# Optimization experiments

Hardware: AMD Instinct MI355X
Metric: run time of the kernel (lower is better)

The kernel has to match this reference:

```python
import jax, jax.numpy as jnp
import numpy as np

K = 1.0      # Lorentz curvature param (geoopt convention: <x,x>_L = -K)
SQK = 1.0    # sqrt(K)
B, LOOKBACK, SEG, D = 256, 4096, 32, 256
N = LOOKBACK // SEG  # 128 segments


def _mink_inner(x, y):
    # Minkowski inner product, keepdims on last axis
    return -x[..., :1] * y[..., :1] + jnp.sum(x[..., 1:] * y[..., 1:], axis=-1, keepdims=True)


def _expmap0_spatial(v):
    # v: [..., D] spatial tangent at origin -> point on hyperboloid [..., D+1]
    n = jnp.linalg.norm(v, axis=-1, keepdims=True)
    ns = jnp.maximum(n, 1e-9)
    x0 = SQK * jnp.cosh(n / SQK)
    xr = SQK * jnp.sinh(n / SQK) * v / ns
    return jnp.concatenate([x0, xr], axis=-1)


def _projx(x):
    # re-project onto hyperboloid: x0 = sqrt(K + ||x_spatial||^2)
    xr = x[..., 1:]
    x0 = jnp.sqrt(K + jnp.sum(xr * xr, axis=-1, keepdims=True))
    return jnp.concatenate([x0, xr], axis=-1)


def _origin_like(x):
    return jnp.zeros_like(x).at[..., 0].set(SQK)


def _logmap(x, y):
    # log_x(y) on the Lorentz manifold
    alpha = jnp.maximum(-_mink_inner(x, y) / K, 1.0 + 1e-7)
    dist = SQK * jnp.arccosh(alpha)
    u = y - alpha * x  # tangent direction (unnormalized)
    un = jnp.sqrt(jnp.maximum(_mink_inner(u, u), 1e-12))
    return dist * u / un


def _expmap(x, u):
    # exp_x(u) on the Lorentz manifold
    un = jnp.sqrt(jnp.maximum(_mink_inner(u, u), 1e-12))
    theta = un / SQK
    return jnp.cosh(theta) * x + jnp.sinh(theta) * SQK * u / un


def _clip_norm(v, max_norm):
    # euclidean-norm clip (torch.norm semantics in source)
    n = jnp.linalg.norm(v, axis=-1, keepdims=True)
    return v / jnp.maximum(n, 1e-12) * jnp.minimum(n, max_norm)


def _encode(x, W, b):
    # [B, lookback] -> [B, N, D]; dropout is identity at eval
    xs = x.reshape(B, N, SEG)
    return jnp.einsum('bns,ds->bnd', xs, W) + b


def _to_hyperbolic(z, effective_scale):
    # vectorized over all segments (original looped over seg_idx)
    v = z * jnp.tanh(effective_scale)
    n = jnp.maximum(jnp.linalg.norm(v, axis=-1, keepdims=True), 1e-8)
    v = v / n * jnp.minimum(n, 1.5)
    return _projx(_expmap0_spatial(v))


def _lorentz_fusion(pts, w):
    # pts: [4, B, N, D+1], w: [4] softmax weights; weighted Karcher mean
    o = _origin_like(pts[0])
    t0 = _logmap(o, pts)                       # tangents at origin (time comp == 0)
    wt = _clip_norm(jnp.einsum('c,cbnd->bnd', w, t0), 2.0)
    mean = _projx(_expmap0_spatial(wt[..., 1:]))  # geoopt expmap0 uses spatial part
    for _ in range(5):                         # fixed 5 Karcher iterations
        tv = _logmap(mean, pts)                # [4, B, N, D+1]
        wv = _clip_norm(jnp.einsum('c,cbnd->bnd', w, tv), 2.0)
        mean = _projx(_expmap(mean, 0.1 * wv))
    return mean


def setup_inputs() -> dict:
    key = jax.random.key(0)
    ks = jax.random.split(key, 12)
    wscale = 1.0 / np.sqrt(SEG)
    inp = {
        'trend': jax.random.normal(ks[0], (B, LOOKBACK), jnp.float32),
        'seasonal_coarse': jax.random.normal(ks[1], (B, LOOKBACK), jnp.float32),
        'seasonal_fine': jax.random.normal(ks[2], (B, LOOKBACK), jnp.float32),
        'residual': jax.random.normal(ks[3], (B, LOOKBACK), jnp.float32),
        'W_trend': jax.random.normal(ks[4], (D, SEG), jnp.float32) * wscale,
        'b_trend': jnp.zeros((D,), jnp.float32),
        'W_coarse': jax.random.normal(ks[5], (D, SEG), jnp.float32) * wscale,
        'b_coarse': jnp.zeros((D,), jnp.float32),
        'W_fine': jax.random.normal(ks[6], (D, SEG), jnp.float32) * wscale,
        'b_fine': jnp.zeros((D,), jnp.float32),
        'W_residual': jax.random.normal(ks[7], (D, SEG), jnp.float32) * wscale,
        'b_residual': jnp.zeros((D,), jnp.float32),
        'effective_scale': jnp.asarray(0.001, jnp.float32),
        'lorentz_weights': jnp.ones((4,), jnp.float32) * 0.25,
    }
    return inp


def reference(trend, seasonal_coarse, seasonal_fine, residual,
              W_trend, b_trend, W_coarse, b_coarse, W_fine, b_fine,
              W_residual, b_residual, effective_scale, lorentz_weights):
    z_t = _encode(trend, W_trend, b_trend)
    z_c = _encode(seasonal_coarse, W_coarse, b_coarse)
    z_f = _encode(seasonal_fine, W_fine, b_fine)
    z_r = _encode(residual, W_residual, b_residual)
    h_t = _to_hyperbolic(z_t, effective_scale)
    h_c = _to_hyperbolic(z_c, effective_scale)
    h_f = _to_hyperbolic(z_f, effective_scale)
    h_r = _to_hyperbolic(z_r, effective_scale)
    w = jax.nn.softmax(lorentz_weights)
    combined = _lorentz_fusion(jnp.stack([h_t, h_c, h_f, h_r], axis=0), w)
    return (h_t, h_c, h_f, h_r, combined)
```

## Files before the change

kernel.cpp:

```cpp
#include <hip/hip_runtime.h>
#include <math.h>

namespace {

typedef float f4 __attribute__((ext_vector_type(4)));

constexpr int PPW  = 4;
constexpr int WPB  = 4;
constexpr int PPB  = PPW * WPB;
constexpr int NPTS = 256 * 128;
constexpr int GRID = NPTS / PPB;
constexpr int OUTS = 257;
constexpr size_t HOFF = (size_t)NPTS * OUTS;
constexpr int LSTR = 260;

__device__ __forceinline__ float frcp(float x)   { return __builtin_amdgcn_rcpf(x); }
__device__ __forceinline__ float fsqrt_(float x) { return __builtin_amdgcn_sqrtf(x); }
__device__ __forceinline__ float facosh(float a) {
  return __logf(a + fsqrt_(fmaf(a, a, -1.f)));
}
__device__ __forceinline__ void fsinhcosh(float x, float& sh, float& ch) {
  float e = __expf(x), ei = frcp(e);
  sh = 0.5f * (e - ei);
  ch = 0.5f * (e + ei);
}
__device__ __forceinline__ float fsinh(float x) {
  float e = __expf(x);
  return 0.5f * (e - frcp(e));
}
__device__ __forceinline__ float dot4(f4 a, f4 b) {
  return a.x * b.x + a.y * b.y + a.z * b.z + a.w * b.w;
}
__device__ __forceinline__ f4 fma4s(float a, f4 b, f4 c) {
  f4 av = {a, a, a, a};
  return __builtin_elementwise_fma(av, b, c);
}

template <int NB>
__device__ __forceinline__ void wave_reduce(float* v) {
#pragma unroll
  for (int off = 32; off > 0; off >>= 1) {
#pragma unroll
    for (int i = 0; i < NB; ++i) v[i] += __shfl_xor(v[i], off, 64);
  }
}

__global__ __launch_bounds__(256) void splmw_kernel(
    const float* __restrict__ xt, const float* __restrict__ xc,
    const float* __restrict__ xf, const float* __restrict__ xr,
    const float* __restrict__ Wt, const float* __restrict__ bt,
    const float* __restrict__ Wc, const float* __restrict__ bc,
    const float* __restrict__ Wf, const float* __restrict__ bf,
    const float* __restrict__ Wr, const float* __restrict__ br,
    const float* __restrict__ esp, const float* __restrict__ lwp,
    float* __restrict__ out) {
  __shared__ float wlds[32 * LSTR];

  const int tid  = threadIdx.x;
  const int lane = tid & 63;
  const int wv   = __builtin_amdgcn_readfirstlane(tid >> 6);
  const int pt0  = blockIdx.x * PPB + wv * PPW;

  float es2 = __expf(2.f * esp[0]);
  const float ts = (es2 - 1.f) * frcp(es2 + 1.f);
  float l0 = lwp[0], l1 = lwp[1], l2 = lwp[2], l3 = lwp[3];
  float mx = fmaxf(fmaxf(l0, l1), fmaxf(l2, l3));
  float e0 = __expf(l0 - mx), e1 = __expf(l1 - mx);
  float e2 = __expf(l2 - mx), e3 = __expf(l3 - mx);
  float ei = frcp(e0 + e1 + e2 + e3);
  const float wgt[4] = {e0 * ei, e1 * ei, e2 * ei, e3 * ei};

  const float* xsarr[4] = {xt, xc, xf, xr};
  const float* Wsarr[4] = {Wt, Wc, Wf, Wr};
  const float* Bsarr[4] = {bt, bc, bf, br};

  f4    h[4][PPW];
  float x0s[4][PPW];
  float r2s[4][PPW];

#pragma unroll
  for (int c = 0; c < 4; ++c) {
    __syncthreads();
    {
      const float* Wp = Wsarr[c];
#pragma unroll
      for (int k = 0; k < 32; ++k) {
        int idx = k * 256 + tid;
        wlds[(idx & 31) * LSTR + (idx >> 5)] = Wp[idx];
      }
    }
    __syncthreads();

    const float* xp = xsarr[c] + (size_t)pt0 * 32;
    {
      f4 bv = ((const f4*)Bsarr[c])[lane];
#pragma unroll
      for (int p = 0; p < PPW; ++p) h[c][p] = bv;
    }
#pragma unroll
    for (int s4 = 0; s4 < 8; ++s4) {
      f4 q0 = *(const f4*)(xp + 4 * s4);
      f4 q1 = *(const f4*)(xp + 32 + 4 * s4);
      f4 q2 = *(const f4*)(xp + 64 + 4 * s4);
      f4 q3 = *(const f4*)(xp + 96 + 4 * s4);
      float xv[4][4] = {{q0.x, q0.y, q0.z, q0.w}, {q1.x, q1.y, q1.z, q1.w},
                        {q2.x, q2.y, q2.z, q2.w}, {q3.x, q3.y, q3.z, q3.w}};
#pragma unroll
      for (int si = 0; si < 4; ++si) {
        int s = 4 * s4 + si;
        f4 w4 = *(const f4*)&wlds[s * LSTR + 4 * lane];
#pragma unroll
        for (int p = 0; p < PPW; ++p) h[c][p] = fma4s(xv[p][si], w4, h[c][p]);
      }
    }

    float pa[PPW];
#pragma unroll
    for (int p = 0; p < PPW; ++p) {
      h[c][p] = ts * h[c][p];
      pa[p]   = dot4(h[c][p], h[c][p]);
    }
    wave_reduce<PPW>(pa);
#pragma unroll
    for (int p = 0; p < PPW; ++p) {
      float n1  = fsqrt_(pa[p]);
      float n1m = fmaxf(n1, 1e-8f);
      float c1  = fminf(n1m, 1.5f) * frcp(n1m);
      float n2  = c1 * n1;
      float nsx = fmaxf(n2, 1e-9f);
      float sh  = fsinh(n2);
      float rn  = frcp(nsx);
      float g   = sh * c1 * rn;
      f4 xq     = g * h[c][p];
      float sxr = sh * n2 * rn;
      float xx0 = fsqrt_(fmaf(sxr, sxr, 1.f));
      h[c][p]   = xq;
      x0s[c][p] = xx0;
      r2s[c][p] = g * g * pa[p];
      float* o = out + (size_t)c * HOFF + (size_t)(pt0 + p) * OUTS;
      if (lane == 0) o[0] = xx0;
      int base = 1 + 4 * lane;
      o[base] = xq.x; o[base + 1] = xq.y; o[base + 2] = xq.z; o[base + 3] = xq.w;
    }
  }

  float wt0[PPW];
  f4    wtr[PPW];
#pragma unroll
  for (int p = 0; p < PPW; ++p) {
    wt0[p] = 0.f;
    wtr[p] = (f4){0.f, 0.f, 0.f, 0.f};
#pragma unroll
    for (int c = 0; c < 4; ++c) {
      float y0    = x0s[c][p];
      float alpha = fmaxf(y0, 1.f + 1e-7f);
      float dist  = facosh(alpha);
      float u0    = y0 - alpha;
      float msq   = r2s[c][p] - u0 * u0;
      float un    = fsqrt_(fmaxf(msq, 1e-12f));
      float f     = wgt[c] * dist * frcp(un);
      wt0[p] = fmaf(f, u0, wt0[p]);
      wtr[p] = fma4s(f, h[c][p], wtr[p]);
    }
  }
  float rrp[PPW];
#pragma unroll
  for (int p = 0; p < PPW; ++p) rrp[p] = dot4(wtr[p], wtr[p]);
  wave_reduce<PPW>(rrp);

  f4    mr[PPW];
  float mrr[PPW], m0[PPW];
#pragma unroll
  for (int p = 0; p < PPW; ++p) {
    float rr  = rrp[p];
    float nrm = fsqrt_(fmaf(wt0[p], wt0[p], rr));
    float scl = fminf(nrm, 2.f) * frcp(fmaxf(nrm, 1e-12f));
    float nr  = scl * fsqrt_(rr);
    float nsx = fmaxf(nr, 1e-9f);
    float g   = fsinh(nr) * scl * frcp(nsx);
    mr[p]  = g * wtr[p];
    mrr[p] = g * g * rr;
    m0[p]  = fsqrt_(1.f + mrr[p]);
  }

#pragma unroll 1
  for (int it = 0; it < 5; ++it) {
    float dots[4 * PPW];
#pragma unroll
    for (int p = 0; p < PPW; ++p)
#pragma unroll
      for (int c = 0; c < 4; ++c) dots[p * 4 + c] = dot4(mr[p], h[c][p]);
    wave_reduce<4 * PPW>(dots);

    float wv0[PPW];
    f4    wvr[PPW];
#pragma unroll
    for (int p = 0; p < PPW; ++p) {
      wv0[p] = 0.f;
      wvr[p] = (f4){0.f, 0.f, 0.f, 0.f};
#pragma unroll
      for (int c = 0; c < 4; ++c) {
        float d     = dots[p * 4 + c];
        float y0    = x0s[c][p];
        float ip    = fmaf(m0[p], y0, -d);
        float alpha = fmaxf(ip, 1.f + 1e-7f);
        float dist  = facosh(alpha);
        float u0    = fmaf(-alpha, m0[p], y0);
        float t   = fmaf(alpha, mrr[p], -2.f * d);
        float s2  = fmaf(alpha, t, r2s[c][p]);
        float msq = s2 - u0 * u0;
        float un  = fsqrt_(fmaxf(msq, 1e-12f));
        float f   = wgt[c] * dist * frcp(un);
        wv0[p] = fmaf(f, u0, wv0[p]);
        f4 diff = fma4s(-alpha, mr[p], h[c][p]);
        wvr[p]  = fma4s(f, diff, wvr[p]);
      }
    }
    float pr[2 * PPW];
#pragma unroll
    for (int p = 0; p < PPW; ++p) {
      pr[p]       = dot4(wvr[p], wvr[p]);
      pr[PPW + p] = dot4(mr[p], wvr[p]);
    }
    wave_reduce<2 * PPW>(pr);

#pragma unroll
    for (int p = 0; p < PPW; ++p) {
      float rr2  = pr[p];
      float mwv  = pr[PPW + p];
      float nrm2 = fsqrt_(fmaf(wv0[p], wv0[p], rr2));
      float sc2  = fminf(nrm2, 2.f) * frcp(fmaxf(nrm2, 1e-12f));
      float tt   = 0.1f * sc2;
      float msqu = tt * tt * (rr2 - wv0[p] * wv0[p]);
      float un2  = fsqrt_(fmaxf(msqu, 1e-12f));
      float shv, chv;
      fsinhcosh(un2, shv, chv);
      float gg = shv * tt * frcp(un2);
      mr[p] = fma4s(chv, mr[p], gg * wvr[p]);
      mrr[p] = chv * chv * mrr[p] + 2.f * chv * gg * mwv + gg * gg * rr2;
      m0[p]  = fsqrt_(1.f + mrr[p]);
    }
  }

#pragma unroll
  for (int p = 0; p < PPW; ++p) {
    float* o = out + 4 * HOFF + (size_t)(pt0 + p) * OUTS;
    if (lane == 0) o[0] = m0[p];
    int base = 1 + 4 * lane;
    f4 v = mr[p];
    o[base] = v.x; o[base + 1] = v.y; o[base + 2] = v.z; o[base + 3] = v.w;
  }
}

}

extern "C" void kernel_launch(void* const* d_in, const int* in_sizes, int n_in,
                              void* d_out, int out_size, void* d_ws, size_t ws_size,
                              hipStream_t stream) {
  (void)in_sizes; (void)n_in; (void)out_size; (void)d_ws; (void)ws_size;
  splmw_kernel<<<GRID, 256, 0, stream>>>(
      (const float*)d_in[0], (const float*)d_in[1], (const float*)d_in[2],
      (const float*)d_in[3], (const float*)d_in[4], (const float*)d_in[5],
      (const float*)d_in[6], (const float*)d_in[7], (const float*)d_in[8],
      (const float*)d_in[9], (const float*)d_in[10], (const float*)d_in[11],
      (const float*)d_in[12], (const float*)d_in[13], (float*)d_out);
}
```

Measured before the change: 319.1 us.

## Map each point to a 16-lane group and vectorize weight transpose loads

Each wavefront now processes four points in parallel, one per 16-lane group, with every lane holding 16 of the 256 features. Before, all 64 lanes shared a single point at a time. Cross-lane reductions shrink from six shuffle stages to four, and the per-point serial loops become one per-lane stream. The weight staging into LDS now uses f4 row loads per thread instead of scalar strided loads. The trade-off is more LDS reads per lane in the GEMV, and the per-lane output writes are now split across four strided chunks.

```diff
diff --git a/kernel.cpp b/kernel.cpp
--- a/kernel.cpp
+++ b/kernel.cpp
@@ -37,9 +37,9 @@
 }
 
 template <int NB>
-__device__ __forceinline__ void wave_reduce(float* v) {
-#pragma unroll
-  for (int off = 32; off > 0; off >>= 1) {
+__device__ __forceinline__ void grp_reduce(float* v) {
+#pragma unroll
+  for (int off = 8; off > 0; off >>= 1) {
 #pragma unroll
     for (int i = 0; i < NB; ++i) v[i] += __shfl_xor(v[i], off, 64);
   }
@@ -58,8 +58,10 @@
 
   const int tid  = threadIdx.x;
   const int lane = tid & 63;
-  const int wv   = __builtin_amdgcn_readfirstlane(tid >> 6);
-  const int pt0  = blockIdx.x * PPB + wv * PPW;
+  const int m    = lane & 15;
+  const int grp  = lane >> 4;
+  const int wv   = tid >> 6;
+  const int pt   = blockIdx.x * PPB + wv * PPW + grp;
 
   float es2 = __expf(2.f * esp[0]);
   const float ts = (es2 - 1.f) * frcp(es2 + 1.f);
@@ -74,56 +76,53 @@
   const float* Wsarr[4] = {Wt, Wc, Wf, Wr};
   const float* Bsarr[4] = {bt, bc, bf, br};
 
-  f4    h[4][PPW];
-  float x0s[4][PPW];
-  float r2s[4][PPW];
+  f4    h[4][4];
+  float x0s[4];
+  float r2s[4];
 
 #pragma unroll
   for (int c = 0; c < 4; ++c) {
+    const float* Wp = Wsarr[c];
+    f4 wrow[8];
+#pragma unroll
+    for (int k = 0; k < 8; ++k) wrow[k] = *(const f4*)(Wp + tid * 32 + 4 * k);
     __syncthreads();
+#pragma unroll
+    for (int k = 0; k < 8; ++k) {
+      wlds[(4 * k + 0) * LSTR + tid] = wrow[k].x;
+      wlds[(4 * k + 1) * LSTR + tid] = wrow[k].y;
+      wlds[(4 * k + 2) * LSTR + tid] = wrow[k].z;
+      wlds[(4 * k + 3) * LSTR + tid] = wrow[k].w;
+    }
+    __syncthreads();
+
+    f4 acc[4];
+    const float* bp = Bsarr[c];
+#pragma unroll
+    for (int j = 0; j < 4; ++j) acc[j] = *(const f4*)(bp + 4 * m + 64 * j);
+    const float* xp = xsarr[c] + (size_t)pt * 32;
+#pragma unroll
+    for (int s4 = 0; s4 < 8; ++s4) {
+      f4 xq = *(const f4*)(xp + 4 * s4);
+      float xa[4] = {xq.x, xq.y, xq.z, xq.w};
+#pragma unroll
+      for (int si = 0; si < 4; ++si) {
+        const float* wr = &wlds[(4 * s4 + si) * LSTR + 4 * m];
+#pragma unroll
+        for (int j = 0; j < 4; ++j)
+          acc[j] = fma4s(xa[si], *(const f4*)(wr + 64 * j), acc[j]);
+      }
+    }
+
+    float pa = 0.f;
+#pragma unroll
+    for (int j = 0; j < 4; ++j) {
+      h[c][j] = ts * acc[j];
+      pa += dot4(h[c][j], h[c][j]);
+    }
+    grp_reduce<1>(&pa);
     {
-      const float* Wp = Wsarr[c];
-#pragma unroll
-      for (int k = 0; k < 32; ++k) {
-        int idx = k * 256 + tid;
-        wlds[(idx & 31) * LSTR + (idx >> 5)] = Wp[idx];
-      }
-    }
-    __syncthreads();
-
-    const float* xp = xsarr[c] + (size_t)pt0 * 32;
-    {
-      f4 bv = ((const f4*)Bsarr[c])[lane];
-#pragma unroll
-      for (int p = 0; p < PPW; ++p) h[c][p] = bv;
-    }
-#pragma unroll
-    for (int s4 = 0; s4 < 8; ++s4) {
-      f4 q0 = *(const f4*)(xp + 4 * s4);
-      f4 q1 = *(const f4*)(xp + 32 + 4 * s4);
-      f4 q2 = *(const f4*)(xp + 64 + 4 * s4);
-      f4 q3 = *(const f4*)(xp + 96 + 4 * s4);
-      float xv[4][4] = {{q0.x, q0.y, q0.z, q0.w}, {q1.x, q1.y, q1.z, q1.w},
-                        {q2.x, q2.y, q2.z, q2.w}, {q3.x, q3.y, q3.z, q3.w}};
-#pragma unroll
-      for (int si = 0; si < 4; ++si) {
-        int s = 4 * s4 + si;
-        f4 w4 = *(const f4*)&wlds[s * LSTR + 4 * lane];
-#pragma unroll
-        for (int p = 0; p < PPW; ++p) h[c][p] = fma4s(xv[p][si], w4, h[c][p]);
-      }
-    }
-
-    float pa[PPW];
-#pragma unroll
-    for (int p = 0; p < PPW; ++p) {
-      h[c][p] = ts * h[c][p];
-      pa[p]   = dot4(h[c][p], h[c][p]);
-    }
-    wave_reduce<PPW>(pa);
-#pragma unroll
-    for (int p = 0; p < PPW; ++p) {
-      float n1  = fsqrt_(pa[p]);
+      float n1  = fsqrt_(pa);
       float n1m = fmaxf(n1, 1e-8f);
       float c1  = fminf(n1m, 1.5f) * frcp(n1m);
       float n2  = c1 * n1;
@@ -131,124 +130,131 @@
       float sh  = fsinh(n2);
       float rn  = frcp(nsx);
       float g   = sh * c1 * rn;
-      f4 xq     = g * h[c][p];
       float sxr = sh * n2 * rn;
       float xx0 = fsqrt_(fmaf(sxr, sxr, 1.f));
-      h[c][p]   = xq;
-      x0s[c][p] = xx0;
-      r2s[c][p] = g * g * pa[p];
-      float* o = out + (size_t)c * HOFF + (size_t)(pt0 + p) * OUTS;
-      if (lane == 0) o[0] = xx0;
-      int base = 1 + 4 * lane;
-      o[base] = xq.x; o[base + 1] = xq.y; o[base + 2] = xq.z; o[base + 3] = xq.w;
-    }
-  }
-
-  float wt0[PPW];
-  f4    wtr[PPW];
-#pragma unroll
-  for (int p = 0; p < PPW; ++p) {
-    wt0[p] = 0.f;
-    wtr[p] = (f4){0.f, 0.f, 0.f, 0.f};
-#pragma unroll
-    for (int c = 0; c < 4; ++c) {
-      float y0    = x0s[c][p];
-      float alpha = fmaxf(y0, 1.f + 1e-7f);
-      float dist  = facosh(alpha);
-      float u0    = y0 - alpha;
-      float msq   = r2s[c][p] - u0 * u0;
-      float un    = fsqrt_(fmaxf(msq, 1e-12f));
-      float f     = wgt[c] * dist * frcp(un);
-      wt0[p] = fmaf(f, u0, wt0[p]);
-      wtr[p] = fma4s(f, h[c][p], wtr[p]);
-    }
-  }
-  float rrp[PPW];
-#pragma unroll
-  for (int p = 0; p < PPW; ++p) rrp[p] = dot4(wtr[p], wtr[p]);
-  wave_reduce<PPW>(rrp);
-
-  f4    mr[PPW];
-  float mrr[PPW], m0[PPW];
-#pragma unroll
-  for (int p = 0; p < PPW; ++p) {
-    float rr  = rrp[p];
-    float nrm = fsqrt_(fmaf(wt0[p], wt0[p], rr));
+#pragma unroll
+      for (int j = 0; j < 4; ++j) h[c][j] = g * h[c][j];
+      x0s[c] = xx0;
+      r2s[c] = g * g * pa;
+      float* o = out + (size_t)c * HOFF + (size_t)pt * OUTS;
+      if (m == 0) o[0] = xx0;
+#pragma unroll
+      for (int j = 0; j < 4; ++j) {
+        int base = 1 + 4 * m + 64 * j;
+        f4 v = h[c][j];
+        o[base] = v.x; o[base + 1] = v.y; o[base + 2] = v.z; o[base + 3] = v.w;
+      }
+    }
+  }
+
+  float wt0 = 0.f;
+  f4    wtr[4];
+#pragma unroll
+  for (int j = 0; j < 4; ++j) wtr[j] = (f4){0.f, 0.f, 0.f, 0.f};
+#pragma unroll
+  for (int c = 0; c < 4; ++c) {
+    float y0    = x0s[c];
+    float alpha = fmaxf(y0, 1.f + 1e-7f);
+    float dist  = facosh(alpha);
+    float u0    = y0 - alpha;
+    float msq   = r2s[c] - u0 * u0;
+    float un    = fsqrt_(fmaxf(msq, 1e-12f));
+    float f     = wgt[c] * dist * frcp(un);
+    wt0 = fmaf(f, u0, wt0);
+#pragma unroll
+    for (int j = 0; j < 4; ++j) wtr[j] = fma4s(f, h[c][j], wtr[j]);
+  }
+  float rrp = 0.f;
+#pragma unroll
+  for (int j = 0; j < 4; ++j) rrp += dot4(wtr[j], wtr[j]);
+  grp_reduce<1>(&rrp);
+
+  f4    mr[4];
+  float mrr, m0;
+  {
+    float rr  = rrp;
+    float nrm = fsqrt_(fmaf(wt0, wt0, rr));
     float scl = fminf(nrm, 2.f) * frcp(fmaxf(nrm, 1e-12f));
     float nr  = scl * fsqrt_(rr);
     float nsx = fmaxf(nr, 1e-9f);
     float g   = fsinh(nr) * scl * frcp(nsx);
-    mr[p]  = g * wtr[p];
-    mrr[p] = g * g * rr;
-    m0[p]  = fsqrt_(1.f + mrr[p]);
+#pragma unroll
+    for (int j = 0; j < 4; ++j) mr[j] = g * wtr[j];
+    mrr = g * g * rr;
+    m0  = fsqrt_(1.f + mrr);
   }
 
 #pragma unroll 1
   for (int it = 0; it < 5; ++it) {
-    float dots[4 * PPW];
-#pragma unroll
-    for (int p = 0; p < PPW; ++p)
-#pragma unroll
-      for (int c = 0; c < 4; ++c) dots[p * 4 + c] = dot4(mr[p], h[c][p]);
-    wave_reduce<4 * PPW>(dots);
-
-    float wv0[PPW];
-    f4    wvr[PPW];
-#pragma unroll
-    for (int p = 0; p < PPW; ++p) {
-      wv0[p] = 0.f;
-      wvr[p] = (f4){0.f, 0.f, 0.f, 0.f};
-#pragma unroll
-      for (int c = 0; c < 4; ++c) {
-        float d     = dots[p * 4 + c];
-        float y0    = x0s[c][p];
-        float ip    = fmaf(m0[p], y0, -d);
-        float alpha = fmaxf(ip, 1.f + 1e-7f);
-        float dist  = facosh(alpha);
-        float u0    = fmaf(-alpha, m0[p], y0);
-        float t   = fmaf(alpha, mrr[p], -2.f * d);
-        float s2  = fmaf(alpha, t, r2s[c][p]);
-        float msq = s2 - u0 * u0;
-        float un  = fsqrt_(fmaxf(msq, 1e-12f));
-        float f   = wgt[c] * dist * frcp(un);
-        wv0[p] = fmaf(f, u0, wv0[p]);
-        f4 diff = fma4s(-alpha, mr[p], h[c][p]);
-        wvr[p]  = fma4s(f, diff, wvr[p]);
+    float dots[4];
+#pragma unroll
+    for (int c = 0; c < 4; ++c) {
+      float d = 0.f;
+#pragma unroll
+      for (int j = 0; j < 4; ++j) d += dot4(mr[j], h[c][j]);
+      dots[c] = d;
+    }
+    grp_reduce<4>(dots);
+
+    float wv0 = 0.f;
+    f4    wvr[4];
+#pragma unroll
+    for (int j = 0; j < 4; ++j) wvr[j] = (f4){0.f, 0.f, 0.f, 0.f};
+#pragma unroll
+    for (int c = 0; c < 4; ++c) {
+      float d     = dots[c];
+      float y0    = x0s[c];
+      float ip    = fmaf(m0, y0, -d);
+      float alpha = fmaxf(ip, 1.f + 1e-7f);
+      float dist  = facosh(alpha);
+      float u0    = fmaf(-alpha, m0, y0);
+      float t   = fmaf(alpha, mrr, -2.f * d);
+      float s2  = fmaf(alpha, t, r2s[c]);
+      float msq = s2 - u0 * u0;
+      float un  = fsqrt_(fmaxf(msq, 1e-12f));
+      float f   = wgt[c] * dist * frcp(un);
+      wv0 = fmaf(f, u0, wv0);
+#pragma unroll
+      for (int j = 0; j < 4; ++j) {
+        f4 diff = fma4s(-alpha, mr[j], h[c][j]);
+        wvr[j]  = fma4s(f, diff, wvr[j]);
       }
     }
-    float pr[2 * PPW];
-#pragma unroll
-    for (int p = 0; p < PPW; ++p) {
-      pr[p]       = dot4(wvr[p], wvr[p]);
-      pr[PPW + p] = dot4(mr[p], wvr[p]);
-    }
-    wave_reduce<2 * PPW>(pr);
-
-#pragma unroll
-    for (int p = 0; p < PPW; ++p) {
-      float rr2  = pr[p];
-      float mwv  = pr[PPW + p];
-      float nrm2 = fsqrt_(fmaf(wv0[p], wv0[p], rr2));
+    float pr[2] = {0.f, 0.f};
+#pragma unroll
+    for (int j = 0; j < 4; ++j) {
+      pr[0] += dot4(wvr[j], wvr[j]);
+      pr[1] += dot4(mr[j], wvr[j]);
+    }
+    grp_reduce<2>(pr);
+
+    {
+      float rr2  = pr[0];
+      float mwv  = pr[1];
+      float nrm2 = fsqrt_(fmaf(wv0, wv0, rr2));
       float sc2  = fminf(nrm2, 2.f) * frcp(fmaxf(nrm2, 1e-12f));
       float tt   = 0.1f * sc2;
-      float msqu = tt * tt * (rr2 - wv0[p] * wv0[p]);
+      float msqu = tt * tt * (rr2 - wv0 * wv0);
       float un2  = fsqrt_(fmaxf(msqu, 1e-12f));
       float shv, chv;
       fsinhcosh(un2, shv, chv);
       float gg = shv * tt * frcp(un2);
-      mr[p] = fma4s(chv, mr[p], gg * wvr[p]);
-      mrr[p] = chv * chv * mrr[p] + 2.f * chv * gg * mwv + gg * gg * rr2;
-      m0[p]  = fsqrt_(1.f + mrr[p]);
-    }
-  }
-
-#pragma unroll
-  for (int p = 0; p < PPW; ++p) {
-    float* o = out + 4 * HOFF + (size_t)(pt0 + p) * OUTS;
-    if (lane == 0) o[0] = m0[p];
-    int base = 1 + 4 * lane;
-    f4 v = mr[p];
-    o[base] = v.x; o[base + 1] = v.y; o[base + 2] = v.z; o[base + 3] = v.w;
+#pragma unroll
+      for (int j = 0; j < 4; ++j) mr[j] = fma4s(chv, mr[j], gg * wvr[j]);
+      mrr = chv * chv * mrr + 2.f * chv * gg * mwv + gg * gg * rr2;
+      m0  = fsqrt_(1.f + mrr);
+    }
+  }
+
+  {
+    float* o = out + 4 * HOFF + (size_t)pt * OUTS;
+    if (m == 0) o[0] = m0;
+#pragma unroll
+    for (int j = 0; j < 4; ++j) {
+      int base = 1 + 4 * m + 64 * j;
+      f4 v = mr[j];
+      o[base] = v.x; o[base + 1] = v.y; o[base + 2] = v.z; o[base + 3] = v.w;
+    }
   }
 }
 
```

After: 276.3 us. 13.4% less time.
